# Kernel optimization log

Hardware: AMD Instinct MI355X
Metric: run time of the kernel (lower is better)

## Reference

```python
import jax, jax.numpy as jnp
import numpy as np

B, T, LZ, D = 8, 4096, 1024, 1024


def setup_inputs() -> dict:
    key = jax.random.key(0)
    k1, k2, k3 = jax.random.split(key, 3)
    z = jax.random.normal(k1, (B, LZ, D), dtype=jnp.float32)
    p = jax.random.uniform(k2, (B, T), dtype=jnp.float32)
    b = jax.random.randint(k3, (B, T), 0, 2, dtype=jnp.int32)
    return {"z": z, "p": p, "b": b, "original_len": T}


def reference(z, p, b, original_len):
    # z: [B, Lz, D], p: [B, T], b: [B, T] in {0,1}
    Lz = z.shape[1]
    # exclusive cumulative sum of boundary flags = run-length chunk index,
    # clamped so that overflow repeats the last chunk (z[:, -1])
    idx = jnp.clip(jnp.cumsum(b, axis=1) - b, 0, Lz - 1)  # [B, T]
    upsampled = jnp.take_along_axis(z, idx[:, :, None], axis=1)  # [B, T, D]
    coef = p[:, :, None]
    rolled = jnp.roll(upsampled, shift=1, axis=1)
    smoothed = coef * upsampled + (1.0 - coef) * rolled
    smoothed = smoothed.at[:, 0].set(upsampled[:, 0])
    return smoothed
```

## Files before the change

kernel.cpp:

```cpp
#include <hip/hip_runtime.h>

#define B_N   8
#define T_N   4096
#define LZ_N  1024
#define D_N   1024
#define ROWS_TOTAL (B_N * T_N)
#define NBLK  2048
#define ROWS_PER_BLK (ROWS_TOTAL / NBLK)

typedef float fx4 __attribute__((ext_vector_type(4)));

__global__ __launch_bounds__(256) void scan_kernel(const int* __restrict__ b,
                                                   int* __restrict__ idx) {
    const int batch = blockIdx.x;
    const int tid   = threadIdx.x;
    const int* bb = b   + (size_t)batch * T_N;
    int*       ii = idx + (size_t)batch * T_N;

    int vals[16];
    const int4* b4 = (const int4*)(bb + tid * 16);
#pragma unroll
    for (int j = 0; j < 4; ++j) {
        int4 v = b4[j];
        vals[4 * j + 0] = v.x;
        vals[4 * j + 1] = v.y;
        vals[4 * j + 2] = v.z;
        vals[4 * j + 3] = v.w;
    }

    int local_sum = 0;
#pragma unroll
    for (int j = 0; j < 16; ++j) local_sum += vals[j];

    __shared__ int sh[256];
    sh[tid] = local_sum;
    __syncthreads();
#pragma unroll
    for (int off = 1; off < 256; off <<= 1) {
        int v = (tid >= off) ? sh[tid - off] : 0;
        __syncthreads();
        sh[tid] += v;
        __syncthreads();
    }
    int excl = (tid == 0) ? 0 : sh[tid - 1];

    int run = excl;
#pragma unroll
    for (int j = 0; j < 16; ++j) {
        int v = run;
        run += vals[j];
        v = v < 0 ? 0 : (v > (LZ_N - 1) ? (LZ_N - 1) : v);
        ii[tid * 16 + j] = v;
    }
}

__global__ __launch_bounds__(256) void smooth_kernel(const float* __restrict__ z,
                                                     const float* __restrict__ p,
                                                     const int* __restrict__ idx,
                                                     float* __restrict__ out) {
    const int bid  = blockIdx.x;
    const int swz  = (bid & 7) * (NBLK / 8) + (bid >> 3);
    const int base = swz * ROWS_PER_BLK;
    const int batch = base >> 12;
    const int tid  = threadIdx.x;

    const float* zb = z + (size_t)batch * LZ_N * D_N;

    const int t0 = base & (T_N - 1);
    int i_prev = (t0 == 0) ? idx[base] : idx[base - 1];
    fx4 v_prev = ((const fx4*)(zb + (size_t)i_prev * D_N))[tid];

    fx4* outp = (fx4*)out + (size_t)base * (D_N / 4) + tid;

#pragma unroll 4
    for (int j = 0; j < ROWS_PER_BLK; ++j) {
        const int row = base + j;
        const int i0  = idx[row];
        fx4 v0;
        if (i0 != i_prev) {
            v0 = ((const fx4*)(zb + (size_t)i0 * D_N))[tid];
        } else {
            v0 = v_prev;
        }
        const float c  = ((row & (T_N - 1)) == 0) ? 1.0f : p[row];
        const float om = 1.0f - c;
        fx4 r = c * v0 + om * v_prev;
        __builtin_nontemporal_store(r, outp + (size_t)j * (D_N / 4));
        i_prev = i0;
        v_prev = v0;
    }
}

extern "C" void kernel_launch(void* const* d_in, const int* in_sizes, int n_in,
                              void* d_out, int out_size, void* d_ws, size_t ws_size,
                              hipStream_t stream) {
    const float* z = (const float*)d_in[0];
    const float* p = (const float*)d_in[1];
    const int*   b = (const int*)d_in[2];

    float* out = (float*)d_out;
    int*   idx = (int*)d_ws;

    scan_kernel<<<B_N, 256, 0, stream>>>(b, idx);
    smooth_kernel<<<NBLK, 256, 0, stream>>>(z, p, idx, out);
}
```

Baseline: 36.06 us.

## Fuse boundary scan into smoothing kernel with per-block redundant prefix sum

Removes the separate scan kernel and its global index buffer. Each smoothing block now recomputes the prefix sum of boundary flags up to its own 16-row tile, using wave shuffles plus a small shared-memory combine, and stages the indices and coefficients in shared memory. This saves a kernel launch and the serial dependency between the two kernels. In exchange, every block redundantly reads up to 4096 flags of its batch and performs the scan itself.

```diff
diff --git a/kernel.cpp b/kernel.cpp
--- a/kernel.cpp
+++ b/kernel.cpp
@@ -10,79 +10,96 @@
 
 typedef float fx4 __attribute__((ext_vector_type(4)));
 
-__global__ __launch_bounds__(256) void scan_kernel(const int* __restrict__ b,
-                                                   int* __restrict__ idx) {
-    const int batch = blockIdx.x;
+__global__ __launch_bounds__(256) void fused_kernel(const float* __restrict__ z,
+                                                    const float* __restrict__ p,
+                                                    const int* __restrict__ b,
+                                                    float* __restrict__ out) {
+    const int bid   = blockIdx.x;
+    const int swz   = (bid & 7) * (NBLK / 8) + (bid >> 3);
+    const int base  = swz * ROWS_PER_BLK;
+    const int batch = base >> 12;
+    const int t0    = base & (T_N - 1);
     const int tid   = threadIdx.x;
-    const int* bb = b   + (size_t)batch * T_N;
-    int*       ii = idx + (size_t)batch * T_N;
+    const int lane  = tid & 63;
+    const int wid   = tid >> 6;
+    const int last_chunk = t0 >> 4;
+    const int nchunk     = last_chunk + 1;
+
+    const int* bb = b + (size_t)batch * T_N;
 
     int vals[16];
-    const int4* b4 = (const int4*)(bb + tid * 16);
+    int lsum = 0;
+    if (tid < nchunk) {
+        const int4* b4 = (const int4*)(bb + tid * 16);
 #pragma unroll
-    for (int j = 0; j < 4; ++j) {
-        int4 v = b4[j];
-        vals[4 * j + 0] = v.x;
-        vals[4 * j + 1] = v.y;
-        vals[4 * j + 2] = v.z;
-        vals[4 * j + 3] = v.w;
+        for (int j = 0; j < 4; ++j) {
+            int4 v = b4[j];
+            vals[4 * j + 0] = v.x;
+            vals[4 * j + 1] = v.y;
+            vals[4 * j + 2] = v.z;
+            vals[4 * j + 3] = v.w;
+        }
+#pragma unroll
+        for (int j = 0; j < 16; ++j) lsum += vals[j];
     }
 
-    int local_sum = 0;
+    int s = lsum;
 #pragma unroll
-    for (int j = 0; j < 16; ++j) local_sum += vals[j];
+    for (int off = 1; off < 64; off <<= 1) {
+        int n = __shfl_up(s, off, 64);
+        if (lane >= off) s += n;
+    }
+    __shared__ int   wsum[4];
+    __shared__ int   sh_idx[17];
+    __shared__ float sh_p[16];
+    if (lane == 63) wsum[wid] = s;
+    __syncthreads();
+    int wbase = 0;
+#pragma unroll
+    for (int w = 0; w < 3; ++w) if (w < wid) wbase += wsum[w];
+    const int incl  = s + wbase;
+    const int exclc = incl - lsum;
 
-    __shared__ int sh[256];
-    sh[tid] = local_sum;
+    if (tid == last_chunk) {
+        int run = exclc;
+        int first = -1;
+#pragma unroll
+        for (int j = 0; j < 16; ++j) {
+            int v = run;
+            run += vals[j];
+            v = v > (LZ_N - 1) ? (LZ_N - 1) : v;
+            if (j == 0) first = v;
+            sh_idx[1 + j] = v;
+        }
+        if (t0 == 0) sh_idx[0] = first;
+    }
+    if (t0 > 0 && tid == last_chunk - 1) {
+        int v = incl - vals[15];
+        v = v > (LZ_N - 1) ? (LZ_N - 1) : v;
+        sh_idx[0] = v;
+    }
+    if (tid < ROWS_PER_BLK) {
+        const int row = base + tid;
+        sh_p[tid] = ((row & (T_N - 1)) == 0) ? 1.0f : p[row];
+    }
     __syncthreads();
-#pragma unroll
-    for (int off = 1; off < 256; off <<= 1) {
-        int v = (tid >= off) ? sh[tid - off] : 0;
-        __syncthreads();
-        sh[tid] += v;
-        __syncthreads();
-    }
-    int excl = (tid == 0) ? 0 : sh[tid - 1];
-
-    int run = excl;
-#pragma unroll
-    for (int j = 0; j < 16; ++j) {
-        int v = run;
-        run += vals[j];
-        v = v < 0 ? 0 : (v > (LZ_N - 1) ? (LZ_N - 1) : v);
-        ii[tid * 16 + j] = v;
-    }
-}
-
-__global__ __launch_bounds__(256) void smooth_kernel(const float* __restrict__ z,
-                                                     const float* __restrict__ p,
-                                                     const int* __restrict__ idx,
-                                                     float* __restrict__ out) {
-    const int bid  = blockIdx.x;
-    const int swz  = (bid & 7) * (NBLK / 8) + (bid >> 3);
-    const int base = swz * ROWS_PER_BLK;
-    const int batch = base >> 12;
-    const int tid  = threadIdx.x;
 
     const float* zb = z + (size_t)batch * LZ_N * D_N;
-
-    const int t0 = base & (T_N - 1);
-    int i_prev = (t0 == 0) ? idx[base] : idx[base - 1];
+    int i_prev = sh_idx[0];
     fx4 v_prev = ((const fx4*)(zb + (size_t)i_prev * D_N))[tid];
 
     fx4* outp = (fx4*)out + (size_t)base * (D_N / 4) + tid;
 
 #pragma unroll 4
     for (int j = 0; j < ROWS_PER_BLK; ++j) {
-        const int row = base + j;
-        const int i0  = idx[row];
+        const int i0 = sh_idx[j + 1];
         fx4 v0;
         if (i0 != i_prev) {
             v0 = ((const fx4*)(zb + (size_t)i0 * D_N))[tid];
         } else {
             v0 = v_prev;
         }
-        const float c  = ((row & (T_N - 1)) == 0) ? 1.0f : p[row];
+        const float c  = sh_p[j];
         const float om = 1.0f - c;
         fx4 r = c * v0 + om * v_prev;
         __builtin_nontemporal_store(r, outp + (size_t)j * (D_N / 4));
@@ -99,8 +116,6 @@
     const int*   b = (const int*)d_in[2];
 
     float* out = (float*)d_out;
-    int*   idx = (int*)d_ws;
 
-    scan_kernel<<<B_N, 256, 0, stream>>>(b, idx);
-    smooth_kernel<<<NBLK, 256, 0, stream>>>(z, p, idx, out);
+    fused_kernel<<<NBLK, 256, 0, stream>>>(z, p, b, out);
 }
```

Result: faster. 32.93 us (-8.7%).
